# Performance work log

Measured on AMD Instinct MI355X. Metric: run time of the kernel, lower is better.

## Reference

```python
import jax, jax.numpy as jnp
import numpy as np

T = 2.0  # temperature from init


def _offdiag(A, n):
    # Row i keeps columns (i+1, ..., i+n-1) mod n  -> shape [n, n-1].
    # Same multiset per row as torch masked_select of the off-diagonal;
    # within-row order differs but the loss is order-invariant.
    cols = (jnp.arange(n)[:, None] + 1 + jnp.arange(n - 1)[None, :]) % n
    return jnp.take_along_axis(A, cols, axis=1)


def setup_inputs() -> dict:
    key = jax.random.key(0)
    k1, k2 = jax.random.split(key)
    features = jax.random.normal(k1, (512, 512), dtype=jnp.float32)
    labels = jax.random.uniform(k2, (512, 1), dtype=jnp.float32) * 10.0
    return {"features": features, "labels": labels}


def reference(features, labels):
    n = features.shape[0]
    # L2-normalize features
    f = features / jnp.linalg.norm(features, axis=-1, keepdims=True)
    # label L1 distance matrix [n, n]
    label_diffs = jnp.abs(labels[:, None, :] - labels[None, :, :]).sum(axis=-1)
    # pairwise L2 feature distance / T (safe sqrt: diagonal is exactly 0)
    diff = f[:, None, :] - f[None, :, :]                    # [n, n, d]
    sq = jnp.sum(diff * diff, axis=-1)                      # [n, n]
    dist = jnp.where(sq > 0, jnp.sqrt(jnp.where(sq > 0, sq, 1.0)), 0.0)
    logits = dist / T
    exp_logits = jnp.exp(logits)
    # drop diagonal -> [n, n-1]
    logits = _offdiag(logits, n)
    exp_logits = _offdiag(exp_logits, n)
    label_diffs = _offdiag(label_diffs, n)
    # rank mask: for anchor i, positive k, negatives j with ld[i,j] >= ld[i,k]
    mask = (label_diffs[:, None, :] >= label_diffs[:, :, None]).astype(features.dtype)  # [n, k, j]
    denom = jnp.einsum('nkj,nj->nk', mask, exp_logits)      # [n, n-1]
    log_probs = logits - jnp.log(denom)                     # [n, n-1]
    loss = -jnp.sum(log_probs) / (n * (n - 1.0))
    return loss
```

## Files before the change

kernel.cpp:

```cpp
#include <hip/hip_runtime.h>
#include <hip/hip_bf16.h>
#include <math.h>


typedef __attribute__((ext_vector_type(8))) short          short8;
typedef __attribute__((ext_vector_type(8))) unsigned short ushort8;
typedef __attribute__((ext_vector_type(4))) float          f32x4;

static __device__ __forceinline__ unsigned short bf16_bits(float f) {
    __hip_bfloat16 h = __float2bfloat16(f);
    return *reinterpret_cast<unsigned short*>(&h);
}

__global__ __launch_bounds__(256) void k_gemm_rank(const float* __restrict__ F,
                                                   const float* __restrict__ labels,
                                                   float* __restrict__ G,
                                                   float* __restrict__ diag,
                                                   float* __restrict__ mlab,
                                                   int* __restrict__ perm,
                                                   int n, int d) {
    const int b = blockIdx.x;
    const int t = threadIdx.x;

    if (b >= 256) {
        __shared__ float ls[512];
        for (int x = t; x < n; x += 256) ls[x] = labels[x];
        __syncthreads();
        const int j = (b - 256) * 256 + t;
        const float lj = ls[j];
        int cnt = 0;
        #pragma unroll 8
        for (int x = 0; x < 512; ++x) {
            float lx = ls[x];
            cnt += (lx < lj) || (lx == lj && x < j);
        }
        mlab[cnt] = lj;
        perm[cnt] = j;
        return;
    }

    __shared__ unsigned short Asm[32][72];
    __shared__ unsigned short Bsm[32][72];

    const int l  = t & 63;
    const int w  = t >> 6;
    const int wr = (w >> 1) << 4;
    const int wc = (w & 1) << 4;

    const int i0 = (b >> 4) << 5;
    const int j0 = (b & 15) << 5;

    const int sr  = t >> 3;
    const int sc8 = (t & 7) << 3;

    const int fr = l & 15;
    const int fk = (l >> 4) << 3;

    const float* pa = &F[(size_t)(i0 + sr) * d + sc8];
    const float* pb = &F[(size_t)(j0 + sr) * d + sc8];

    float4 a0 = *(const float4*)(pa + 0), a1 = *(const float4*)(pa + 4);
    float4 b0 = *(const float4*)(pb + 0), b1 = *(const float4*)(pb + 4);

    f32x4 acc = {};

    for (int k0 = 0; k0 < d; k0 += 64) {
        ushort8 va, vb;
        va[0] = bf16_bits(a0.x); va[1] = bf16_bits(a0.y);
        va[2] = bf16_bits(a0.z); va[3] = bf16_bits(a0.w);
        va[4] = bf16_bits(a1.x); va[5] = bf16_bits(a1.y);
        va[6] = bf16_bits(a1.z); va[7] = bf16_bits(a1.w);
        vb[0] = bf16_bits(b0.x); vb[1] = bf16_bits(b0.y);
        vb[2] = bf16_bits(b0.z); vb[3] = bf16_bits(b0.w);
        vb[4] = bf16_bits(b1.x); vb[5] = bf16_bits(b1.y);
        vb[6] = bf16_bits(b1.z); vb[7] = bf16_bits(b1.w);
        *(ushort8*)&Asm[sr][sc8] = va;
        *(ushort8*)&Bsm[sr][sc8] = vb;
        __syncthreads();

        const int kn = (k0 + 64 < d) ? k0 + 64 : k0;
        a0 = *(const float4*)(pa + kn + 0); a1 = *(const float4*)(pa + kn + 4);
        b0 = *(const float4*)(pb + kn + 0); b1 = *(const float4*)(pb + kn + 4);

        #pragma unroll
        for (int ks = 0; ks < 2; ++ks) {
            short8 af = *(const short8*)&Asm[wr + fr][ks * 32 + fk];
            short8 bf = *(const short8*)&Bsm[wc + fr][ks * 32 + fk];
            acc = __builtin_amdgcn_mfma_f32_16x16x32_bf16(af, bf, acc, 0, 0, 0);
        }
        __syncthreads();
    }

    const int orow = (l >> 4) << 2;
    #pragma unroll
    for (int r = 0; r < 4; ++r) {
        int gi = i0 + wr + orow + r;
        int gj = j0 + wc + fr;
        float v = acc[r];
        G[(size_t)gi * n + gj] = v;
        if (gi == gj) diag[gi] = v;
    }
}

__global__ __launch_bounds__(256) void k_loss(const float* __restrict__ labels,
                                              const float* __restrict__ G,
                                              const float* __restrict__ diag,
                                              const float* __restrict__ mlab,
                                              const int* __restrict__ perm,
                                              float* __restrict__ row_sums,
                                              int n) {
    const int i    = blockIdx.x;
    const int t    = threadIdx.x;
    const int lane = t & 63;
    const int w    = t >> 6;

    __shared__ float m_s[512];
    __shared__ int   pm_s[512];
    __shared__ float dg_s[512];
    __shared__ float g_s[512];
    __shared__ float sc[512];
    __shared__ float wtot[4];
    __shared__ float red[4];
    __shared__ int   p_s;

    const float* Grow = G + (size_t)i * n;

    {
        float2 mv = ((const float2*)mlab)[t];
        int2   pv = ((const int2*)perm)[t];
        float2 dv = ((const float2*)diag)[t];
        float2 gv = ((const float2*)Grow)[t];
        m_s[2 * t] = mv.x;  m_s[2 * t + 1] = mv.y;
        pm_s[2 * t] = pv.x; pm_s[2 * t + 1] = pv.y;
        dg_s[2 * t] = dv.x; dg_s[2 * t + 1] = dv.y;
        g_s[2 * t] = gv.x;  g_s[2 * t + 1] = gv.y;
    }
    const float li = labels[i];
    const float di = diag[i];
    __syncthreads();

    float lgt[2], Dk[2], ev[2];
    int   jn[2];
    #pragma unroll
    for (int qq = 0; qq < 2; ++qq) {
        const int q = 2 * t + qq;
        const int j = pm_s[q];
        jn[qq] = j;
        float gq = g_s[j];
        float sq = fmaxf(2.f - 2.f * gq * rsqrtf(di * dg_s[j]), 0.f);
        float lg = 0.5f * sqrtf(sq);
        lgt[qq] = lg;
        ev[qq]  = (j == i) ? 0.f : __expf(lg);
        Dk[qq]  = fabsf(m_s[q] - li);
        if (j == i) p_s = q;
    }

    {
        float ps = ev[0] + ev[1];
        #pragma unroll
        for (int m = 1; m < 64; m <<= 1) {
            float v = __shfl_up(ps, m);
            if (lane >= m) ps += v;
        }
        if (lane == 63) wtot[w] = ps;
        __syncthreads();
        float woff = 0.f;
        #pragma unroll
        for (int w2 = 0; w2 < 4; ++w2) woff += (w2 < w) ? wtot[w2] : 0.f;
        float inc1 = woff + ps;
        sc[2 * t]     = inc1 - ev[1];
        sc[2 * t + 1] = inc1;
        __syncthreads();
    }
    const float tot = wtot[0] + wtot[1] + wtot[2] + wtot[3];
    const int p = p_s;

    float acc = 0.f;
    #pragma unroll
    for (int qq = 0; qq < 2; ++qq) {
        if (jn[qq] == i) continue;
        const float D = Dk[qq];
        int lo = 0, hi = p + 1;
        while (lo < hi) {
            int mid = (lo + hi) >> 1;
            if (fabsf(m_s[mid] - li) >= D) lo = mid + 1; else hi = mid;
        }
        const int cL = lo;
        lo = p; hi = n;
        while (lo < hi) {
            int mid = (lo + hi) >> 1;
            if (fabsf(m_s[mid] - li) >= D) hi = mid; else lo = mid + 1;
        }
        const int rI = lo;
        float S = (cL > 0 ? sc[cL - 1] : 0.f) + tot - (rI > 0 ? sc[rI - 1] : 0.f);
        acc += lgt[qq] - __logf(S);
    }

    #pragma unroll
    for (int off = 32; off > 0; off >>= 1) acc += __shfl_down(acc, off);
    if (lane == 0) red[w] = acc;
    __syncthreads();
    if (t == 0) row_sums[i] = red[0] + red[1] + red[2] + red[3];
}

__global__ __launch_bounds__(256) void k_final(const float* __restrict__ row_sums,
                                               float* __restrict__ out, int n) {
    const int t = threadIdx.x;
    __shared__ float red[4];
    float s = 0.f;
    for (int r = t; r < n; r += 256) s += row_sums[r];
    #pragma unroll
    for (int off = 32; off > 0; off >>= 1) s += __shfl_down(s, off);
    const int lane = t & 63, w = t >> 6;
    if (lane == 0) red[w] = s;
    __syncthreads();
    if (t == 0) {
        float tot = red[0] + red[1] + red[2] + red[3];
        out[0] = -tot / ((float)n * ((float)n - 1.0f));
    }
}

extern "C" void kernel_launch(void* const* d_in, const int* in_sizes, int n_in,
                              void* d_out, int out_size, void* d_ws, size_t ws_size,
                              hipStream_t stream) {
    const float* F      = (const float*)d_in[0];
    const float* labels = (const float*)d_in[1];
    int n = in_sizes[1];
    int d = in_sizes[0] / n;
    float* out = (float*)d_out;

    char* ws = (char*)d_ws;
    float* row_sums   = (float*)(ws + 4096);
    float* diag       = (float*)(ws + 8192);
    float* mlab       = (float*)(ws + 12288);
    int*   perm       = (int*)(ws + 14336);
    float* G          = (float*)(ws + 16384);

    k_gemm_rank<<<258, 256, 0, stream>>>(F, labels, G, diag, mlab, perm, n, d);
    k_loss<<<n, 256, 0, stream>>>(labels, G, diag, mlab, perm, row_sums, n);
    k_final<<<1, 256, 0, stream>>>(row_sums, out, n);
}
```

Before: 27.38 us.

## Load full K panels into swizzled LDS once instead of per-k-step pipeline

The GEMM kernel now loads each block's entire 32x512 A and B panels into LDS in one batch of 16 unrolled float4 loads, converts them to bf16, and stores them with an XOR swizzle to avoid bank conflicts. It then runs all 16 MFMA steps with no intermediate barriers. This removes the per-k-step syncthreads and register-prefetch loop, exposing more memory-level parallelism. In exchange it uses 64KB of LDS per block, which limits occupancy, and it hardcodes d=512.

```diff
diff --git a/kernel.cpp b/kernel.cpp
--- a/kernel.cpp
+++ b/kernel.cpp
@@ -4,7 +4,7 @@
 
 
 typedef __attribute__((ext_vector_type(8))) short          short8;
-typedef __attribute__((ext_vector_type(8))) unsigned short ushort8;
+typedef __attribute__((ext_vector_type(4))) unsigned short ushort4v;
 typedef __attribute__((ext_vector_type(4))) float          f32x4;
 
 static __device__ __forceinline__ unsigned short bf16_bits(float f) {
@@ -19,11 +19,14 @@
                                                    float* __restrict__ mlab,
                                                    int* __restrict__ perm,
                                                    int n, int d) {
+    __shared__ unsigned short Asm[32][512];
+    __shared__ unsigned short Bsm[32][512];
+
     const int b = blockIdx.x;
     const int t = threadIdx.x;
 
     if (b >= 256) {
-        __shared__ float ls[512];
+        float* ls = (float*)&Asm[0][0];
         for (int x = t; x < n; x += 256) ls[x] = labels[x];
         __syncthreads();
         const int j = (b - 256) * 256 + t;
@@ -39,9 +42,6 @@
         return;
     }
 
-    __shared__ unsigned short Asm[32][72];
-    __shared__ unsigned short Bsm[32][72];
-
     const int l  = t & 63;
     const int w  = t >> 6;
     const int wr = (w >> 1) << 4;
@@ -50,45 +50,38 @@
     const int i0 = (b >> 4) << 5;
     const int j0 = (b & 15) << 5;
 
-    const int sr  = t >> 3;
-    const int sc8 = (t & 7) << 3;
-
     const int fr = l & 15;
     const int fk = (l >> 4) << 3;
 
-    const float* pa = &F[(size_t)(i0 + sr) * d + sc8];
-    const float* pb = &F[(size_t)(j0 + sr) * d + sc8];
-
-    float4 a0 = *(const float4*)(pa + 0), a1 = *(const float4*)(pa + 4);
-    float4 b0 = *(const float4*)(pb + 0), b1 = *(const float4*)(pb + 4);
-
+    #pragma unroll
+    for (int p = 0; p < 16; ++p) {
+        const int idx = p * 1024 + t * 4;
+        const int row = idx >> 9;
+        const int col = idx & 511;
+        float4 av = *(const float4*)&F[(size_t)(i0 + row) * 512 + col];
+        float4 bv = *(const float4*)&F[(size_t)(j0 + row) * 512 + col];
+        ushort4v ua, ub;
+        ua[0] = bf16_bits(av.x); ua[1] = bf16_bits(av.y);
+        ua[2] = bf16_bits(av.z); ua[3] = bf16_bits(av.w);
+        ub[0] = bf16_bits(bv.x); ub[1] = bf16_bits(bv.y);
+        ub[2] = bf16_bits(bv.z); ub[3] = bf16_bits(bv.w);
+        const int cu = col ^ ((row & 7) << 3);
+        *(ushort4v*)&Asm[row][cu] = ua;
+        *(ushort4v*)&Bsm[row][cu] = ub;
+    }
+    __syncthreads();
+
+    const int rA = wr + fr;
+    const int rB = wc + fr;
+    const int sxA = (rA & 7) << 3;
+    const int sxB = (rB & 7) << 3;
     f32x4 acc = {};
-
-    for (int k0 = 0; k0 < d; k0 += 64) {
-        ushort8 va, vb;
-        va[0] = bf16_bits(a0.x); va[1] = bf16_bits(a0.y);
-        va[2] = bf16_bits(a0.z); va[3] = bf16_bits(a0.w);
-        va[4] = bf16_bits(a1.x); va[5] = bf16_bits(a1.y);
-        va[6] = bf16_bits(a1.z); va[7] = bf16_bits(a1.w);
-        vb[0] = bf16_bits(b0.x); vb[1] = bf16_bits(b0.y);
-        vb[2] = bf16_bits(b0.z); vb[3] = bf16_bits(b0.w);
-        vb[4] = bf16_bits(b1.x); vb[5] = bf16_bits(b1.y);
-        vb[6] = bf16_bits(b1.z); vb[7] = bf16_bits(b1.w);
-        *(ushort8*)&Asm[sr][sc8] = va;
-        *(ushort8*)&Bsm[sr][sc8] = vb;
-        __syncthreads();
-
-        const int kn = (k0 + 64 < d) ? k0 + 64 : k0;
-        a0 = *(const float4*)(pa + kn + 0); a1 = *(const float4*)(pa + kn + 4);
-        b0 = *(const float4*)(pb + kn + 0); b1 = *(const float4*)(pb + kn + 4);
-
-        #pragma unroll
-        for (int ks = 0; ks < 2; ++ks) {
-            short8 af = *(const short8*)&Asm[wr + fr][ks * 32 + fk];
-            short8 bf = *(const short8*)&Bsm[wc + fr][ks * 32 + fk];
-            acc = __builtin_amdgcn_mfma_f32_16x16x32_bf16(af, bf, acc, 0, 0, 0);
-        }
-        __syncthreads();
+    #pragma unroll
+    for (int ks = 0; ks < 16; ++ks) {
+        const int colk = ks * 32 + fk;
+        short8 af = *(const short8*)&Asm[rA][colk ^ sxA];
+        short8 bf = *(const short8*)&Bsm[rB][colk ^ sxB];
+        acc = __builtin_amdgcn_mfma_f32_16x16x32_bf16(af, bf, acc, 0, 0, 0);
     }
 
     const int orow = (l >> 4) << 2;
```

New measurement: 25.91 us, median of 2. 5.4% less time.
